# Kernel tuning notes

Hardware: AMD Instinct MI355X
Metric: run time of the kernel (lower is better)

## Reference

```python
import jax, jax.numpy as jnp
import numpy as np

N = 8192          # num_nodes
F_IN = 512        # num_features
D = 256           # embedding_dim
C = 40            # num_classes
E = 262144        # num_edges (avg degree 32)
ALPHA = 0.5
LN_EPS = 1e-5


def _layer_norm(x, eps=LN_EPS):
    # F.layer_norm over last dim, no affine params
    mu = jnp.mean(x, axis=-1, keepdims=True)
    var = jnp.var(x, axis=-1, keepdims=True)
    return (x - mu) * jax.lax.rsqrt(var + eps)


def setup_inputs() -> dict:
    key = jax.random.key(0)
    ks = jax.random.split(key, 16)
    s_in = 1.0 / np.sqrt(F_IN)
    s_d = 1.0 / np.sqrt(D)
    inp = {
        "X": jax.random.normal(ks[0], (N, F_IN), dtype=jnp.float32),
        "edge_row": jnp.sort(jax.random.randint(ks[1], (E,), 0, N)),
        "edge_col": jax.random.randint(ks[2], (E,), 0, N),
        "edge_weight": jax.random.uniform(ks[3], (E,), dtype=jnp.float32),
        # MLP embedding: Linear(F_IN, D)
        "W_emb": jax.random.uniform(ks[4], (F_IN, D), minval=-s_in, maxval=s_in),
        "b_emb": jax.random.uniform(ks[5], (D,), minval=-s_in, maxval=s_in),
        # attention projections: Linear(D, D) x3
        "W_q": jax.random.uniform(ks[6], (D, D), minval=-s_d, maxval=s_d),
        "b_q": jax.random.uniform(ks[7], (D,), minval=-s_d, maxval=s_d),
        "W_k": jax.random.uniform(ks[8], (D, D), minval=-s_d, maxval=s_d),
        "b_k": jax.random.uniform(ks[9], (D,), minval=-s_d, maxval=s_d),
        "W_v": jax.random.uniform(ks[10], (D, D), minval=-s_d, maxval=s_d),
        "b_v": jax.random.uniform(ks[11], (D,), minval=-s_d, maxval=s_d),
        # GNN linear: Linear(D, D)
        "W_gnn": jax.random.uniform(ks[12], (D, D), minval=-s_d, maxval=s_d),
        "b_gnn": jax.random.uniform(ks[13], (D,), minval=-s_d, maxval=s_d),
        # classifier: Linear(D, C)
        "W_cls": jax.random.uniform(ks[14], (D, C), minval=-s_d, maxval=s_d),
        "b_cls": jax.random.uniform(ks[15], (C,), minval=-s_d, maxval=s_d),
    }
    return inp


def reference(X, edge_row, edge_col, edge_weight,
              W_emb, b_emb, W_q, b_q, W_k, b_k, W_v, b_v,
              W_gnn, b_gnn, W_cls, b_cls):
    # embedding MLP
    Z0 = X @ W_emb + b_emb                      # [N, D]
    # global attention with QK layer-norm
    Q = _layer_norm(Z0 @ W_q + b_q)             # [N, D]
    K = _layer_norm(Z0 @ W_k + b_k)             # [N, D]
    V = Z0 @ W_v + b_v                          # [N, D]
    scores = Q @ K.T                            # [N, N]
    attn = jax.nn.softmax(scores, axis=-1)      # [N, N]
    Z_A = attn @ V                              # [N, D]
    # sparse GNN branch: spmm(A, linear(Z0))
    H = Z0 @ W_gnn + b_gnn                      # [N, D]
    msg = H[edge_col] * edge_weight[:, None]    # [E, D]
    gnn_out = jax.ops.segment_sum(msg, edge_row, num_segments=N)  # [N, D]
    # weighted blend + classifier
    Z_out = (1.0 - ALPHA) * Z_A + ALPHA * gnn_out
    Y_hat = Z_out @ W_cls + b_cls               # [N, C]
    return (Y_hat, attn)
```

## Files before the change

kernel.cpp:

```cpp
#include <hip/hip_runtime.h>
#include <hip/hip_bf16.h>

#define N_NODES 8192
#define F_IN    512
#define DIM     256
#define NCLS    40

typedef __attribute__((ext_vector_type(8))) short bf16x8;
typedef __attribute__((ext_vector_type(4))) float f32x4;

#define MFMA16 __builtin_amdgcn_mfma_f32_16x16x32_bf16

static __device__ __forceinline__ unsigned short f2bf(float x) {
    __hip_bfloat16 h = __float2bfloat16(x);
    return *reinterpret_cast<unsigned short*>(&h);
}
static __device__ __forceinline__ float bf2f(unsigned short u) {
    union { unsigned int u32; float f; } v; v.u32 = ((unsigned int)u) << 16;
    return v.f;
}
static __device__ __forceinline__ void gll16(const void* g, void* l) {
    __builtin_amdgcn_global_load_lds(
        (const __attribute__((address_space(1))) unsigned int*)g,
        (__attribute__((address_space(3))) unsigned int*)l, 16, 0, 0);
}

__global__ __launch_bounds__(256) void split_kernel(
    const float* __restrict__ X,
    unsigned short* __restrict__ Xh, unsigned short* __restrict__ Xl)
{
    const size_t i = ((size_t)blockIdx.x * 256 + threadIdx.x) * 4;
    float4 v = *(const float4*)&X[i];
    ushort4 h, l;
    h.x = f2bf(v.x); l.x = f2bf(v.x - bf2f(h.x));
    h.y = f2bf(v.y); l.y = f2bf(v.y - bf2f(h.y));
    h.z = f2bf(v.z); l.z = f2bf(v.z - bf2f(h.z));
    h.w = f2bf(v.w); l.w = f2bf(v.w - bf2f(h.w));
    *(ushort4*)&Xh[i] = h;
    *(ushort4*)&Xl[i] = l;
}

__global__ __launch_bounds__(256) void wtrans_kernel(
    const float* __restrict__ W,
    unsigned short* __restrict__ WTh, unsigned short* __restrict__ WTl,
    int K, int N)
{
    __shared__ float tile[64][65];
    const int r0 = blockIdx.x * 64;
    const int c0 = blockIdx.y * 64;
    const int t = threadIdx.x;
    #pragma unroll
    for (int i = 0; i < 4; ++i) {
        int r = i * 16 + (t >> 4);
        int c = (t & 15) * 4;
        float4 v = *(const float4*)&W[(size_t)(r0 + r) * N + c0 + c];
        tile[r][c] = v.x; tile[r][c + 1] = v.y;
        tile[r][c + 2] = v.z; tile[r][c + 3] = v.w;
    }
    __syncthreads();
    #pragma unroll
    for (int i = 0; i < 4; ++i) {
        int c = i * 16 + (t >> 4);
        int r = (t & 15) * 4;
        ushort4 h, l;
        float x0 = tile[r][c],     x1 = tile[r + 1][c];
        float x2 = tile[r + 2][c], x3 = tile[r + 3][c];
        h.x = f2bf(x0); l.x = f2bf(x0 - bf2f(h.x));
        h.y = f2bf(x1); l.y = f2bf(x1 - bf2f(h.y));
        h.z = f2bf(x2); l.z = f2bf(x2 - bf2f(h.z));
        h.w = f2bf(x3); l.w = f2bf(x3 - bf2f(h.w));
        *(ushort4*)&WTh[(size_t)(c0 + c) * K + r0 + r] = h;
        *(ushort4*)&WTl[(size_t)(c0 + c) * K + r0 + r] = l;
    }
}

template<int KDIM, int OUTMODE>
__device__ __forceinline__ void gemm3_body(
    const unsigned short* __restrict__ Ah_, const unsigned short* __restrict__ Al_,
    const unsigned short* __restrict__ Bh_, const unsigned short* __restrict__ Bl_,
    const float* __restrict__ bias,
    void* __restrict__ C0, void* __restrict__ C1,
    int m0, int n0,
    short (*Ah)[32], short (*Al)[32], short (*Bh)[32], short (*Bl)[32])
{
    const int t = threadIdx.x, lane = t & 63, w = t >> 6;
    const int wm = w >> 1, wn = w & 1;
    const int fr = lane & 15, kb = lane >> 4;

    const unsigned short* asrc[4];
    const unsigned short* bsrc[4];
    char* adst[4];
    char* bdst[4];
    #pragma unroll
    for (int r = 0; r < 4; ++r) {
        int c = r * 256 + t;
        int tens = c >> 9, idx = c & 511;
        int row = idx >> 2, slot = idx & 3;
        asrc[r] = (tens ? Al_ : Ah_) + (size_t)(m0 + row) * KDIM + slot * 8;
        adst[r] = (char*)(tens ? &Al[0][0] : &Ah[0][0]) + idx * 16;
        bsrc[r] = (tens ? Bl_ : Bh_) + (size_t)(n0 + row) * KDIM + slot * 8;
        bdst[r] = (char*)(tens ? &Bl[0][0] : &Bh[0][0]) + idx * 16;
    }

    f32x4 acc[4][4] = {};

    for (int k0 = 0; k0 < KDIM; k0 += 32) {
        #pragma unroll
        for (int r = 0; r < 4; ++r) { gll16(asrc[r], adst[r]); asrc[r] += 32; }
        #pragma unroll
        for (int r = 0; r < 4; ++r) { gll16(bsrc[r], bdst[r]); bsrc[r] += 32; }
        __syncthreads();

        bf16x8 ah[4], al[4], bh[4], bl[4];
        #pragma unroll
        for (int m = 0; m < 4; ++m) {
            int row = wm * 64 + m * 16 + fr;
            ah[m] = *(const bf16x8*)&Ah[row][kb * 8];
            al[m] = *(const bf16x8*)&Al[row][kb * 8];
        }
        #pragma unroll
        for (int n = 0; n < 4; ++n) {
            int col = wn * 64 + n * 16 + fr;
            bh[n] = *(const bf16x8*)&Bh[col][kb * 8];
            bl[n] = *(const bf16x8*)&Bl[col][kb * 8];
        }
        #pragma unroll
        for (int m = 0; m < 4; ++m)
            #pragma unroll
            for (int n = 0; n < 4; ++n) {
                acc[m][n] = MFMA16(ah[m], bh[n], acc[m][n], 0, 0, 0);
                acc[m][n] = MFMA16(ah[m], bl[n], acc[m][n], 0, 0, 0);
                acc[m][n] = MFMA16(al[m], bh[n], acc[m][n], 0, 0, 0);
            }
        __syncthreads();
    }

    #pragma unroll
    for (int m = 0; m < 4; ++m)
        #pragma unroll
        for (int e = 0; e < 4; ++e) {
            const int row = m0 + wm * 64 + m * 16 + kb * 4 + e;
            #pragma unroll
            for (int n = 0; n < 4; ++n) {
                const int col = n0 + wn * 64 + n * 16 + fr;
                float v = acc[m][n][e] + bias[col];
                if (OUTMODE == 0) {
                    ((float*)C0)[(size_t)row * 256 + col] = v;
                } else if (OUTMODE == 1) {
                    ((unsigned short*)C0)[(size_t)row * 256 + col] = f2bf(v);
                } else {
                    unsigned short h = f2bf(v);
                    ((unsigned short*)C0)[(size_t)row * 256 + col] = h;
                    ((unsigned short*)C1)[(size_t)row * 256 + col] =
                        f2bf(v - bf2f(h));
                }
            }
        }
}

template<int KDIM, int OUTMODE>
__global__ __launch_bounds__(256, 2) void mfma_gemm3_kernel(
    const unsigned short* __restrict__ Ah_, const unsigned short* __restrict__ Al_,
    const unsigned short* __restrict__ Bh_, const unsigned short* __restrict__ Bl_,
    const float* __restrict__ bias,
    void* __restrict__ C0, void* __restrict__ C1)
{
    __shared__ short Ah[128][32], Al[128][32], Bh[128][32], Bl[128][32];
    gemm3_body<KDIM, OUTMODE>(Ah_, Al_, Bh_, Bl_, bias, C0, C1,
                              blockIdx.y * 128, blockIdx.x * 128,
                              Ah, Al, Bh, Bl);
}

struct Proj4Args {
    const unsigned short* Bh[4];
    const unsigned short* Bl[4];
    const float* bias[4];
    void* C[4];
};

__global__ __launch_bounds__(256, 2) void proj4_kernel(
    const unsigned short* __restrict__ Ah_, const unsigned short* __restrict__ Al_,
    Proj4Args p)
{
    __shared__ short Ah[128][32], Al[128][32], Bh[128][32], Bl[128][32];
    const int z = blockIdx.z;
    if (z < 3)
        gemm3_body<DIM, 0>(Ah_, Al_, p.Bh[z], p.Bl[z], p.bias[z], p.C[z],
                           nullptr, blockIdx.y * 128, blockIdx.x * 128,
                           Ah, Al, Bh, Bl);
    else
        gemm3_body<DIM, 1>(Ah_, Al_, p.Bh[z], p.Bl[z], p.bias[z], p.C[z],
                           nullptr, blockIdx.y * 128, blockIdx.x * 128,
                           Ah, Al, Bh, Bl);
}

__global__ __launch_bounds__(256) void ln_split_kernel(
    const float* __restrict__ X,
    unsigned short* __restrict__ Hi, unsigned short* __restrict__ Lo)
{
    const int row = blockIdx.x;
    const int t = threadIdx.x;
    float x = X[(size_t)row * DIM + t];

    float s1 = x, s2 = x * x;
    #pragma unroll
    for (int o = 32; o; o >>= 1) {
        s1 += __shfl_xor(s1, o);
        s2 += __shfl_xor(s2, o);
    }
    __shared__ float r1[4], r2[4];
    const int wid = t >> 6;
    if ((t & 63) == 0) { r1[wid] = s1; r2[wid] = s2; }
    __syncthreads();
    const float sum = r1[0] + r1[1] + r1[2] + r1[3];
    const float ssq = r2[0] + r2[1] + r2[2] + r2[3];
    const float mean = sum * (1.0f / DIM);
    const float var  = ssq * (1.0f / DIM) - mean * mean;
    const float y = (x - mean) * rsqrtf(var + 1e-5f);

    const unsigned short h = f2bf(y);
    Hi[(size_t)row * DIM + t] = h;
    Lo[(size_t)row * DIM + t] = f2bf(y - bf2f(h));
}

__global__ __launch_bounds__(256) void vtrans_kernel(
    const float* __restrict__ V, unsigned short* __restrict__ VT)
{
    __shared__ float tile[64][65];
    const int r0 = blockIdx.x * 64;
    const int c0 = blockIdx.y * 64;
    const int t = threadIdx.x;
    #pragma unroll
    for (int i = 0; i < 4; ++i) {
        int r = i * 16 + (t >> 4);
        int c = (t & 15) * 4;
        float4 v = *(const float4*)&V[(size_t)(r0 + r) * DIM + c0 + c];
        tile[r][c] = v.x; tile[r][c + 1] = v.y;
        tile[r][c + 2] = v.z; tile[r][c + 3] = v.w;
    }
    __syncthreads();
    #pragma unroll
    for (int i = 0; i < 4; ++i) {
        int c = i * 16 + (t >> 4);
        int r = (t & 15) * 4;
        ushort4 o;
        o.x = f2bf(tile[r][c]);     o.y = f2bf(tile[r + 1][c]);
        o.z = f2bf(tile[r + 2][c]); o.w = f2bf(tile[r + 3][c]);
        *(ushort4*)&VT[(size_t)(c0 + c) * N_NODES + r0 + r] = o;
    }
}

__global__ __launch_bounds__(256, 4) void qkt_kernel(
    const unsigned short* __restrict__ Qh, const unsigned short* __restrict__ Ql,
    const unsigned short* __restrict__ Kh, const unsigned short* __restrict__ Kl,
    unsigned short* __restrict__ Sb, float2* __restrict__ pstat)
{
    __shared__ short stage[4][128][32];
    __shared__ float2 ps[2][128];
    __shared__ float gmr[128];

    const int bid = blockIdx.x;
    const int x   = bid & 7;
    const int i   = bid >> 3;
    const int nbs = i >> 6;
    const int j   = i & 63;
    const int mb  = x * 8 + (j & 7);
    const int nb  = nbs * 8 + (j >> 3);
    const int m0 = mb * 128, n0 = nb * 128;

    const int t = threadIdx.x, lane = t & 63, w = t >> 6;
    const int wm = w >> 1, wn = w & 1;
    const int fr = lane & 15, kb = lane >> 4;

    const unsigned short* qsrc[2][2];
    const unsigned short* ksrc[2][2];
    char* qdst[2][2];
    char* kdst[2][2];
    #pragma unroll
    for (int r = 0; r < 2; ++r) {
        int c = r * 256 + t;
        int row = c >> 2, slot = c & 3;
        size_t ga = (size_t)(m0 + row) * DIM + slot * 8;
        size_t gb = (size_t)(n0 + row) * DIM + slot * 8;
        qsrc[r][0] = Qh + ga; qsrc[r][1] = Ql + ga;
        ksrc[r][0] = Kh + gb; ksrc[r][1] = Kl + gb;
        qdst[r][0] = (char*)&stage[0][0][0] + c * 16;
        qdst[r][1] = (char*)&stage[1][0][0] + c * 16;
        kdst[r][0] = (char*)&stage[2][0][0] + c * 16;
        kdst[r][1] = (char*)&stage[3][0][0] + c * 16;
    }

    f32x4 acc[4][4] = {};

    for (int k0 = 0; k0 < DIM; k0 += 32) {
        #pragma unroll
        for (int r = 0; r < 2; ++r) {
            gll16(qsrc[r][0], qdst[r][0]); qsrc[r][0] += 32;
            gll16(qsrc[r][1], qdst[r][1]); qsrc[r][1] += 32;
            gll16(ksrc[r][0], kdst[r][0]); ksrc[r][0] += 32;
            gll16(ksrc[r][1], kdst[r][1]); ksrc[r][1] += 32;
        }
        __syncthreads();

        bf16x8 ah[4], al[4], bh[4], bl[4];
        #pragma unroll
        for (int m = 0; m < 4; ++m) {
            int row = wm * 64 + m * 16 + fr;
            ah[m] = *(const bf16x8*)&stage[0][row][kb * 8];
            al[m] = *(const bf16x8*)&stage[1][row][kb * 8];
        }
        #pragma unroll
        for (int n = 0; n < 4; ++n) {
            int col = wn * 64 + n * 16 + fr;
            bh[n] = *(const bf16x8*)&stage[2][col][kb * 8];
            bl[n] = *(const bf16x8*)&stage[3][col][kb * 8];
        }
        #pragma unroll
        for (int m = 0; m < 4; ++m)
            #pragma unroll
            for (int n = 0; n < 4; ++n) {
                acc[m][n] = MFMA16(ah[m], bh[n], acc[m][n], 0, 0, 0);
                acc[m][n] = MFMA16(ah[m], bl[n], acc[m][n], 0, 0, 0);
                acc[m][n] = MFMA16(al[m], bh[n], acc[m][n], 0, 0, 0);
            }
        __syncthreads();
    }

    #pragma unroll
    for (int m = 0; m < 4; ++m)
        #pragma unroll
        for (int e = 0; e < 4; ++e) {
            float mx = acc[m][0][e];
            #pragma unroll
            for (int n = 1; n < 4; ++n) mx = fmaxf(mx, acc[m][n][e]);
            #pragma unroll
            for (int o = 1; o < 16; o <<= 1) mx = fmaxf(mx, __shfl_xor(mx, o));
            if (fr == 0) ps[wn][wm * 64 + m * 16 + kb * 4 + e].x = mx;
        }
    __syncthreads();
    if (t < 128) gmr[t] = fmaxf(ps[0][t].x, ps[1][t].x);
    __syncthreads();

    unsigned short* tile = (unsigned short*)&stage[0][0][0];
    #pragma unroll
    for (int m = 0; m < 4; ++m)
        #pragma unroll
        for (int e = 0; e < 4; ++e) {
            const int rl = wm * 64 + m * 16 + kb * 4 + e;
            const float g = gmr[rl];
            const int key = kb << 1;
            float se = 0.f;
            #pragma unroll
            for (int n = 0; n < 4; ++n) {
                float ev = __expf(acc[m][n][e] - g);
                se += ev;
                const int col = wn * 64 + n * 16 + fr;
                tile[rl * 128 + (((col >> 3) ^ key) << 3) + (col & 7)] =
                    f2bf(ev);
            }
            #pragma unroll
            for (int o = 1; o < 16; o <<= 1) se += __shfl_xor(se, o);
            if (fr == 0) ps[wn][rl].y = se;
        }
    __syncthreads();
    if (t < 128)
        pstat[(size_t)(m0 + t) * 64 + nb] =
            make_float2(gmr[t], ps[0][t].y + ps[1][t].y);

    #pragma unroll
    for (int p = 0; p < 8; ++p) {
        int c = p * 256 + t;
        int r = c >> 4, sl = c & 15;
        int slx = sl ^ (((r >> 2) & 3) << 1);
        *(int4*)&Sb[(size_t)(m0 + r) * 16384 + n0 + sl * 8] =
            *(const int4*)((const char*)tile + (r * 16 + slx) * 16);
    }
}

__global__ __launch_bounds__(256) void factor_kernel(
    const float2* __restrict__ pstat, float* __restrict__ factab)
{
    const int row = blockIdx.x * 4 + (threadIdx.x >> 6);
    const int lane = threadIdx.x & 63;
    float2 v = pstat[(size_t)row * 64 + lane];
    float gm = v.x;
    #pragma unroll
    for (int o = 1; o < 64; o <<= 1) gm = fmaxf(gm, __shfl_xor(gm, o));
    float s = v.y * __expf(v.x - gm);
    #pragma unroll
    for (int o = 1; o < 64; o <<= 1) s += __shfl_xor(s, o);
    factab[(size_t)row * 64 + lane] = __expf(v.x - gm) / s;
}

__global__ __launch_bounds__(256, 2) void av_mfma_kernel(
    const unsigned short* __restrict__ Sb, const float* __restrict__ factab,
    const unsigned short* __restrict__ VT,
    float* __restrict__ P0, float* __restrict__ P1,
    float* __restrict__ P2, float* __restrict__ P3)
{
    __shared__ unsigned short As[2][64][128];
    __shared__ float facsT[16][64];

    const int bid = blockIdx.x;
    const int x = bid & 7, i = bid >> 3;
    const int ks = i >> 4;
    const int rb = (i & 15) * 8 + x;
    const int r0 = rb * 64, kbase = ks * 2048, cb0 = ks * 16;
    const int t = threadIdx.x, lane = t & 63, w = t >> 6;
    const int fr = lane & 15, kb = lane >> 4;

    for (int ii = t; ii < 1024; ii += 256)
        facsT[ii >> 6][ii & 63] =
            factab[(size_t)(r0 + (ii & 63)) * 64 + cb0 + (ii >> 6)];

    const unsigned short* vb[4];
    #pragma unroll
    for (int n = 0; n < 4; ++n)
        vb[n] = VT + (size_t)(w * 64 + n * 16 + fr) * N_NODES + kbase + kb * 8;

    const unsigned short* ssrc[4];
    char* sdst[4];
    #pragma unroll
    for (int p = 0; p < 4; ++p) {
        int c = p * 256 + t;
        int rr = c >> 4, sl = c & 15;
        int slp = sl ^ (rr & 7);
        ssrc[p] = Sb + (size_t)(r0 + rr) * 16384 + kbase + slp * 8;
        sdst[p] = (char*)&As[0][0][0] + c * 16;
    }

    #define STAGE(BUF_) do {                                                  \
        _Pragma("unroll")                                                     \
        for (int p = 0; p < 4; ++p) {                                         \
            gll16(ssrc[p], sdst[p] + (BUF_) * 16384);                         \
            ssrc[p] += 128;                                                   \
        } } while (0)

    f32x4 acc[4][4] = {};
    const f32x4 z4 = {0.f, 0.f, 0.f, 0.f};

    STAGE(0);
    __syncthreads();

    for (int s = 0; s < 16; ++s) {
        const int b = s & 1;
        if (s + 1 < 16) STAGE(b ^ 1);

        bf16x8 bb[4][4];
        #pragma unroll
        for (int ksl = 0; ksl < 4; ++ksl)
            #pragma unroll
            for (int n = 0; n < 4; ++n)
                bb[ksl][n] = *(const bf16x8*)(vb[n] + s * 128 + ksl * 32);

        const char* abase = (const char*)&As[b][0][0];
        #pragma unroll
        for (int m = 0; m < 4; ++m) {
            f32x4 sacc[4];
            {
                bf16x8 a = *(const bf16x8*)(abase + (m * 16 + fr) * 256 +
                                            ((kb ^ (fr & 7)) * 16));
                #pragma unroll
                for (int n = 0; n < 4; ++n)
                    sacc[n] = MFMA16(a, bb[0][n], z4, 0, 0, 0);
            }
            #pragma unroll
            for (int ksl = 1; ksl < 4; ++ksl) {
                bf16x8 a = *(const bf16x8*)(abase + (m * 16 + fr) * 256 +
                                            (((ksl * 4 + kb) ^ (fr & 7)) * 16));
                #pragma unroll
                for (int n = 0; n < 4; ++n)
                    sacc[n] = MFMA16(a, bb[ksl][n], sacc[n], 0, 0, 0);
            }
            f32x4 fac = *(const f32x4*)&facsT[s][m * 16 + kb * 4];
            #pragma unroll
            for (int n = 0; n < 4; ++n)
                acc[m][n] += fac * sacc[n];
        }
        __syncthreads();
    }
    #undef STAGE

    float* P = (ks == 0) ? P0 : (ks == 1) ? P1 : (ks == 2) ? P2 : P3;
    #pragma unroll
    for (int m = 0; m < 4; ++m)
        #pragma unroll
        for (int e = 0; e < 4; ++e) {
            int row = r0 + m * 16 + kb * 4 + e;
            #pragma unroll
            for (int n = 0; n < 4; ++n)
                P[(size_t)row * DIM + w * 64 + n * 16 + fr] = acc[m][n][e];
        }
}

__global__ __launch_bounds__(256) void scale_kernel(
    const unsigned short* __restrict__ Sb, const float* __restrict__ factab,
    float* __restrict__ attn)
{
    const int row = blockIdx.x;
    const int t = threadIdx.x;
    const unsigned short* src = Sb + (size_t)row * 16384;

    int4 v[4];
    float f[4];
    #pragma unroll
    for (int p = 0; p < 4; ++p) {
        int c = p * 256 + t;
        v[p] = *(const int4*)&src[c * 8];
        f[p] = factab[(size_t)row * 64 + (c >> 4)];
    }
    __syncthreads();

    float* dst = attn + (size_t)row * N_NODES;
    #pragma unroll
    for (int p = 0; p < 4; ++p) {
        int c = p * 256 + t;
        float4 o0, o1;
        o0.x = bf2f((unsigned short)(v[p].x & 0xffff)) * f[p];
        o0.y = bf2f((unsigned short)((unsigned)v[p].x >> 16)) * f[p];
        o0.z = bf2f((unsigned short)(v[p].y & 0xffff)) * f[p];
        o0.w = bf2f((unsigned short)((unsigned)v[p].y >> 16)) * f[p];
        o1.x = bf2f((unsigned short)(v[p].z & 0xffff)) * f[p];
        o1.y = bf2f((unsigned short)((unsigned)v[p].z >> 16)) * f[p];
        o1.z = bf2f((unsigned short)(v[p].w & 0xffff)) * f[p];
        o1.w = bf2f((unsigned short)((unsigned)v[p].w >> 16)) * f[p];
        *(float4*)(dst + c * 8)     = o0;
        *(float4*)(dst + c * 8 + 4) = o1;
    }
}

__global__ __launch_bounds__(256) void spmm_kernel(
    const unsigned short* __restrict__ Hb, const int* __restrict__ erow,
    const int* __restrict__ ecol, const float* __restrict__ ew,
    float* __restrict__ out, int E)
{
    const int node = blockIdx.x * 4 + (threadIdx.x >> 6);
    const int lane = threadIdx.x & 63;

    int lo = 0, hi = E;
    while (lo < hi) { int mid = (lo + hi) >> 1; if (erow[mid] < node) lo = mid + 1; else hi = mid; }
    const int beg = lo;
    hi = E;
    while (lo < hi) { int mid = (lo + hi) >> 1; if (erow[mid] < node + 1) lo = mid + 1; else hi = mid; }
    const int end = lo;

    float4 acc = make_float4(0.f, 0.f, 0.f, 0.f);
    for (int e = beg; e < end; ++e) {
        const int col = ecol[e];
        const float wgt = ew[e];
        ushort4 h = *(const ushort4*)&Hb[(size_t)col * DIM + lane * 4];
        acc.x += wgt * bf2f(h.x);
        acc.y += wgt * bf2f(h.y);
        acc.z += wgt * bf2f(h.z);
        acc.w += wgt * bf2f(h.w);
    }
    *(float4*)&out[(size_t)node * DIM + lane * 4] = acc;
}

__global__ __launch_bounds__(256) void blend_cls_kernel(
    const float* __restrict__ p0, const float* __restrict__ p1,
    const float* __restrict__ p2, const float* __restrict__ p3,
    const float* __restrict__ gnn,
    const float* __restrict__ Wc, const float* __restrict__ bc,
    float* __restrict__ Y)
{
    const int row = blockIdx.x;
    const int t = threadIdx.x;
    __shared__ float z[DIM];
    __shared__ float part[4][NCLS];

    const size_t i = (size_t)row * DIM + t;
    z[t] = 0.5f * (p0[i] + p1[i] + p2[i] + p3[i] + gnn[i]);
    __syncthreads();

    if (t < 160) {
        const int c = t % NCLS, q = t / NCLS;
        float acc = 0.0f;
        #pragma unroll 4
        for (int d = q * 64; d < q * 64 + 64; ++d)
            acc += z[d] * Wc[d * NCLS + c];
        part[q][c] = acc;
    }
    __syncthreads();
    if (t < NCLS)
        Y[(size_t)row * NCLS + t] =
            part[0][t] + part[1][t] + part[2][t] + part[3][t] + bc[t];
}

extern "C" void kernel_launch(void* const* d_in, const int* in_sizes, int n_in,
                              void* d_out, int out_size, void* d_ws, size_t ws_size,
                              hipStream_t stream)
{
    const float* X     = (const float*)d_in[0];
    const int*   erow  = (const int*)d_in[1];
    const int*   ecol  = (const int*)d_in[2];
    const float* ew    = (const float*)d_in[3];
    const float* W_emb = (const float*)d_in[4];
    const float* b_emb = (const float*)d_in[5];
    const float* W_q   = (const float*)d_in[6];
    const float* b_q   = (const float*)d_in[7];
    const float* W_k   = (const float*)d_in[8];
    const float* b_k   = (const float*)d_in[9];
    const float* W_v   = (const float*)d_in[10];
    const float* b_v   = (const float*)d_in[11];
    const float* W_g   = (const float*)d_in[12];
    const float* b_g   = (const float*)d_in[13];
    const float* W_c   = (const float*)d_in[14];
    const float* b_c   = (const float*)d_in[15];
    const int E = in_sizes[1];

    float* Y    = (float*)d_out;
    float* Sc   = Y + (size_t)N_NODES * NCLS;
    unsigned short* Sb = (unsigned short*)Sc;

    const size_t ND = (size_t)N_NODES * DIM;
    float* R0 = (float*)d_ws;
    float* R1 = R0 + ND;
    float* R2 = R1 + ND;
    float* R3 = R2 + ND;
    float* R4 = R3 + ND;
    float* R5 = R4 + ND;
    float* R6 = R5 + ND;

    unsigned short* Xh = (unsigned short*)R0;
    unsigned short* Xl = (unsigned short*)R1;
    unsigned short* Wt = (unsigned short*)R2;
    unsigned short* WembTh = Wt;
    unsigned short* WembTl = Wt + 256 * 512;
    unsigned short* WqTh = WembTl + 256 * 512;
    unsigned short* WqTl = WqTh + 256 * 256;
    unsigned short* WkTh = WqTl + 256 * 256;
    unsigned short* WkTl = WkTh + 256 * 256;
    unsigned short* WvTh = WkTl + 256 * 256;
    unsigned short* WvTl = WvTh + 256 * 256;
    unsigned short* WgTh = WvTl + 256 * 256;
    unsigned short* WgTl = WgTh + 256 * 256;
    unsigned short* Z0h = (unsigned short*)R3;
    unsigned short* Z0l = Z0h + ND;
    float* Qf = R4;
    float* Kf = R5;
    float* Vf = R6;
    unsigned short* Hb = (unsigned short*)R0;
    unsigned short* Qh = (unsigned short*)R1;
    unsigned short* Ql = Qh + ND;
    unsigned short* Kh = (unsigned short*)R2;
    unsigned short* Kl = Kh + ND;
    unsigned short* VT = (unsigned short*)(R0 + ND / 2);
    float2* pstat = (float2*)R4;
    float*  factab = R5;
    float* P0 = R6;
    float* P1 = R3;
    float* P2 = R4;
    float* P3 = R1;
    float* GNN = R2;

    split_kernel<<<(N_NODES * F_IN) / 1024, 256, 0, stream>>>(X, Xh, Xl);

    wtrans_kernel<<<dim3(F_IN / 64, DIM / 64), 256, 0, stream>>>(W_emb, WembTh, WembTl, F_IN, DIM);
    wtrans_kernel<<<dim3(DIM / 64, DIM / 64), 256, 0, stream>>>(W_q, WqTh, WqTl, DIM, DIM);
    wtrans_kernel<<<dim3(DIM / 64, DIM / 64), 256, 0, stream>>>(W_k, WkTh, WkTl, DIM, DIM);
    wtrans_kernel<<<dim3(DIM / 64, DIM / 64), 256, 0, stream>>>(W_v, WvTh, WvTl, DIM, DIM);
    wtrans_kernel<<<dim3(DIM / 64, DIM / 64), 256, 0, stream>>>(W_g, WgTh, WgTl, DIM, DIM);

    mfma_gemm3_kernel<F_IN, 2><<<dim3(2, N_NODES / 128), 256, 0, stream>>>(
        Xh, Xl, WembTh, WembTl, b_emb, Z0h, Z0l);

    Proj4Args pa;
    pa.Bh[0] = WqTh; pa.Bl[0] = WqTl; pa.bias[0] = b_q; pa.C[0] = Qf;
    pa.Bh[1] = WkTh; pa.Bl[1] = WkTl; pa.bias[1] = b_k; pa.C[1] = Kf;
    pa.Bh[2] = WvTh; pa.Bl[2] = WvTl; pa.bias[2] = b_v; pa.C[2] = Vf;
    pa.Bh[3] = WgTh; pa.Bl[3] = WgTl; pa.bias[3] = b_g; pa.C[3] = Hb;
    proj4_kernel<<<dim3(2, N_NODES / 128, 4), 256, 0, stream>>>(Z0h, Z0l, pa);

    ln_split_kernel<<<N_NODES, 256, 0, stream>>>(Qf, Qh, Ql);
    ln_split_kernel<<<N_NODES, 256, 0, stream>>>(Kf, Kh, Kl);

    vtrans_kernel<<<dim3(N_NODES / 64, DIM / 64), 256, 0, stream>>>(Vf, VT);

    qkt_kernel<<<4096, 256, 0, stream>>>(Qh, Ql, Kh, Kl, Sb, pstat);

    factor_kernel<<<N_NODES / 4, 256, 0, stream>>>(pstat, factab);

    av_mfma_kernel<<<512, 256, 0, stream>>>(Sb, factab, VT, P0, P1, P2, P3);

    scale_kernel<<<N_NODES, 256, 0, stream>>>(Sb, factab, Sc);

    spmm_kernel<<<N_NODES / 4, 256, 0, stream>>>(Hb, erow, ecol, ew, GNN, E);

    blend_cls_kernel<<<N_NODES, 256, 0, stream>>>(
        P0, P1, P2, P3, GNN, W_c, b_c, Y);
}
```

Before: 429.8 us.

## Fuse attention-probability scaling into AV kernel using in-place bf16 staging layout

The separate scale kernel, which re-read the bf16 score matrix and wrote fp32 attention, is removed. Its work now happens inside the AV MFMA kernel, which scales the score tiles it already holds in LDS and writes attn directly. The bf16 scores are stored in the upper half of each 4096-short segment, apparently so the buffer can alias the fp32 attn output. The fp32 writes then trail the bf16 reads within each segment. This saves a full pass over the score matrix and one kernel launch. The cost is extra store traffic inside the MFMA loop and a correctness dependency on the write and read ordering.

New measurement: 411.6 us. -4.2%, faster.

```diff
diff --git a/kernel.cpp b/kernel.cpp
--- a/kernel.cpp
+++ b/kernel.cpp
@@ -267,6 +267,7 @@
     const int mb  = x * 8 + (j & 7);
     const int nb  = nbs * 8 + (j >> 3);
     const int m0 = mb * 128, n0 = nb * 128;
+    const int sbbase = (nb >> 4) * 4096 + 2048 + (nb & 15) * 128;
 
     const int t = threadIdx.x, lane = t & 63, w = t >> 6;
     const int wm = w >> 1, wn = w & 1;
@@ -372,7 +373,7 @@
         int c = p * 256 + t;
         int r = c >> 4, sl = c & 15;
         int slx = sl ^ (((r >> 2) & 3) << 1);
-        *(int4*)&Sb[(size_t)(m0 + r) * 16384 + n0 + sl * 8] =
+        *(int4*)&Sb[(size_t)(m0 + r) * 16384 + sbbase + sl * 8] =
             *(const int4*)((const char*)tile + (r * 16 + slx) * 16);
     }
 }
@@ -394,7 +395,7 @@
 
 __global__ __launch_bounds__(256, 2) void av_mfma_kernel(
     const unsigned short* __restrict__ Sb, const float* __restrict__ factab,
-    const unsigned short* __restrict__ VT,
+    const unsigned short* __restrict__ VT, float* __restrict__ attn,
     float* __restrict__ P0, float* __restrict__ P1,
     float* __restrict__ P2, float* __restrict__ P3)
 {
@@ -425,7 +426,7 @@
         int c = p * 256 + t;
         int rr = c >> 4, sl = c & 15;
         int slp = sl ^ (rr & 7);
-        ssrc[p] = Sb + (size_t)(r0 + rr) * 16384 + kbase + slp * 8;
+        ssrc[p] = Sb + (size_t)(r0 + rr) * 16384 + ks * 4096 + 2048 + slp * 8;
         sdst[p] = (char*)&As[0][0][0] + c * 16;
     }
 
@@ -477,6 +478,27 @@
             for (int n = 0; n < 4; ++n)
                 acc[m][n] += fac * sacc[n];
         }
+
+        #pragma unroll
+        for (int p = 0; p < 4; ++p) {
+            int ci = p * 256 + t;
+            int rr = ci >> 4, g = ci & 15;
+            const float fac = facsT[s][rr];
+            int4 v = *(const int4*)(abase + (rr * 16 + (g ^ (rr & 7))) * 16);
+            float* dst = attn + (size_t)(r0 + rr) * N_NODES +
+                         kbase + s * 128 + g * 8;
+            float4 o0, o1;
+            o0.x = bf2f((unsigned short)(v.x & 0xffff)) * fac;
+            o0.y = bf2f((unsigned short)((unsigned)v.x >> 16)) * fac;
+            o0.z = bf2f((unsigned short)(v.y & 0xffff)) * fac;
+            o0.w = bf2f((unsigned short)((unsigned)v.y >> 16)) * fac;
+            o1.x = bf2f((unsigned short)(v.z & 0xffff)) * fac;
+            o1.y = bf2f((unsigned short)((unsigned)v.z >> 16)) * fac;
+            o1.z = bf2f((unsigned short)(v.w & 0xffff)) * fac;
+            o1.w = bf2f((unsigned short)((unsigned)v.w >> 16)) * fac;
+            *(float4*)dst       = o0;
+            *(float4*)(dst + 4) = o1;
+        }
         __syncthreads();
     }
     #undef STAGE
@@ -491,42 +513,6 @@
             for (int n = 0; n < 4; ++n)
                 P[(size_t)row * DIM + w * 64 + n * 16 + fr] = acc[m][n][e];
         }
-}
-
-__global__ __launch_bounds__(256) void scale_kernel(
-    const unsigned short* __restrict__ Sb, const float* __restrict__ factab,
-    float* __restrict__ attn)
-{
-    const int row = blockIdx.x;
-    const int t = threadIdx.x;
-    const unsigned short* src = Sb + (size_t)row * 16384;
-
-    int4 v[4];
-    float f[4];
-    #pragma unroll
-    for (int p = 0; p < 4; ++p) {
-        int c = p * 256 + t;
-        v[p] = *(const int4*)&src[c * 8];
-        f[p] = factab[(size_t)row * 64 + (c >> 4)];
-    }
-    __syncthreads();
-
-    float* dst = attn + (size_t)row * N_NODES;
-    #pragma unroll
-    for (int p = 0; p < 4; ++p) {
-        int c = p * 256 + t;
-        float4 o0, o1;
-        o0.x = bf2f((unsigned short)(v[p].x & 0xffff)) * f[p];
-        o0.y = bf2f((unsigned short)((unsigned)v[p].x >> 16)) * f[p];
-        o0.z = bf2f((unsigned short)(v[p].y & 0xffff)) * f[p];
-        o0.w = bf2f((unsigned short)((unsigned)v[p].y >> 16)) * f[p];
-        o1.x = bf2f((unsigned short)(v[p].z & 0xffff)) * f[p];
-        o1.y = bf2f((unsigned short)((unsigned)v[p].z >> 16)) * f[p];
-        o1.z = bf2f((unsigned short)(v[p].w & 0xffff)) * f[p];
-        o1.w = bf2f((unsigned short)((unsigned)v[p].w >> 16)) * f[p];
-        *(float4*)(dst + c * 8)     = o0;
-        *(float4*)(dst + c * 8 + 4) = o1;
-    }
 }
 
 __global__ __launch_bounds__(256) void spmm_kernel(
@@ -681,9 +667,8 @@
 
     factor_kernel<<<N_NODES / 4, 256, 0, stream>>>(pstat, factab);
 
-    av_mfma_kernel<<<512, 256, 0, stream>>>(Sb, factab, VT, P0, P1, P2, P3);
-
-    scale_kernel<<<N_NODES, 256, 0, stream>>>(Sb, factab, Sc);
+    av_mfma_kernel<<<512, 256, 0, stream>>>(
+        Sb, factab, VT, Sc, P0, P1, P2, P3);
 
     spmm_kernel<<<N_NODES / 4, 256, 0, stream>>>(Hb, erow, ecol, ew, GNN, E);
 
```
